# Kernel tuning notes

Hardware: AMD Instinct MI355X
Metric: run time of the kernel (lower is better)

The kernel has to match this reference:

```python
import jax, jax.numpy as jnp
import numpy as np

N = 50000
E = 800000
IN_DIM = 128
HIDDEN = 128
OUT_DIM = 64
NUM_GRAPHS = 64


def setup_inputs() -> dict:
    key = jax.random.key(0)
    ks = jax.random.split(key, 16)
    x = jax.random.normal(ks[0], (N, IN_DIM), dtype=jnp.float32)
    edge_index = jax.random.randint(ks[1], (2, E), 0, N, dtype=jnp.int32)
    batch = jnp.sort(jax.random.randint(ks[2], (N,), 0, NUM_GRAPHS, dtype=jnp.int32))

    def glorot(k, shape):
        fan_in = shape[1]
        return jax.random.normal(k, shape, dtype=jnp.float32) / jnp.sqrt(jnp.float32(fan_in))

    # SAGEConv params: lin_l (on aggregated neighbors, with bias), lin_r (on self, no bias)
    return {
        "x": x,
        "edge_index": edge_index,
        "batch": batch,
        "W1l": glorot(ks[3], (HIDDEN, IN_DIM)), "b1l": jnp.zeros((HIDDEN,), jnp.float32),
        "W1r": glorot(ks[4], (HIDDEN, IN_DIM)),
        "W2l": glorot(ks[5], (HIDDEN, HIDDEN)), "b2l": jnp.zeros((HIDDEN,), jnp.float32),
        "W2r": glorot(ks[6], (HIDDEN, HIDDEN)),
        "W3l": glorot(ks[7], (HIDDEN, HIDDEN)), "b3l": jnp.zeros((HIDDEN,), jnp.float32),
        "W3r": glorot(ks[8], (HIDDEN, HIDDEN)),
        "Wlin": glorot(ks[9], (OUT_DIM, HIDDEN)), "blin": jnp.zeros((OUT_DIM,), jnp.float32),
    }


def sage_conv(x, src, dst, Wl, bl, Wr):
    # aggr='add': scatter-add source features onto target nodes, then two linears.
    agg = jax.ops.segment_sum(x[src], dst, num_segments=N)  # [N, d_in]
    return agg @ Wl.T + bl + x @ Wr.T


def reference(x, edge_index, batch, W1l, b1l, W1r, W2l, b2l, W2r, W3l, b3l, W3r, Wlin, blin):
    src, dst = edge_index[0], edge_index[1]
    h = jax.nn.relu(sage_conv(x, src, dst, W1l, b1l, W1r))
    # dropout p=0.3 is identity at inference
    h = jax.nn.relu(sage_conv(h, src, dst, W2l, b2l, W2r))
    h = sage_conv(h, src, dst, W3l, b3l, W3r)
    # global mean pool over graphs
    sums = jax.ops.segment_sum(h, batch, num_segments=NUM_GRAPHS)  # [G, hidden]
    counts = jax.ops.segment_sum(jnp.ones((N,), h.dtype), batch, num_segments=NUM_GRAPHS)
    pooled = sums / jnp.maximum(counts, 1.0)[:, None]
    return pooled @ Wlin.T + blin  # [G, out_dim]
```

## Files before the change

kernel.cpp:

```cpp
#include <hip/hip_runtime.h>


typedef __bf16 bf16x8 __attribute__((ext_vector_type(8)));
typedef float f32x4 __attribute__((ext_vector_type(4)));
typedef float f32x2 __attribute__((ext_vector_type(2)));

#define BINB 160
#define NBMAX 512

static __device__ __forceinline__ float bf2f(unsigned short u) {
    union { unsigned u; float f; } c; c.u = (unsigned)u << 16; return c.f;
}
static __device__ __forceinline__ unsigned short f2bf(float f) {
    unsigned u = __builtin_bit_cast(unsigned, f);
    return (unsigned short)((u + 0x7fffu + ((u >> 16) & 1u)) >> 16);
}
static __device__ __forceinline__ uint2 pk8_fp8(const float* f) {
    int lo = 0, hi = 0;
    lo = __builtin_amdgcn_cvt_pk_fp8_f32(f[0], f[1], lo, false);
    lo = __builtin_amdgcn_cvt_pk_fp8_f32(f[2], f[3], lo, true);
    hi = __builtin_amdgcn_cvt_pk_fp8_f32(f[4], f[5], hi, false);
    hi = __builtin_amdgcn_cvt_pk_fp8_f32(f[6], f[7], hi, true);
    return make_uint2((unsigned)lo, (unsigned)hi);
}
static __device__ __forceinline__ unsigned char f2fp8(float v) {
    return (unsigned char)(__builtin_amdgcn_cvt_pk_fp8_f32(v, v, 0, false) & 0xff);
}

__global__ __launch_bounds__(256) void k_bincount(
    const int* __restrict__ dst, int* __restrict__ cnt_mat, int E, int nb, int epb)
{
    __shared__ int lc[NBMAX];
    for (int i = threadIdx.x; i < nb; i += 256) lc[i] = 0;
    __syncthreads();
    int b0 = blockIdx.x * epb;
    int b1 = min(b0 + epb, E);
    for (int i = b0 + threadIdx.x; i < b1; i += 256)
        atomicAdd(&lc[dst[i] >> 7], 1);
    __syncthreads();
    for (int i = threadIdx.x; i < nb; i += 256)
        cnt_mat[i * BINB + blockIdx.x] = lc[i];
}

__global__ __launch_bounds__(256) void k_mrowscan(
    const int* __restrict__ cnt_mat, int* __restrict__ rowloc, int* __restrict__ btot)
{
    __shared__ int s[256];
    int b = blockIdx.x;
    int t = threadIdx.x;
    int v = (t < BINB) ? cnt_mat[b * BINB + t] : 0;
    s[t] = v;
    __syncthreads();
#pragma unroll
    for (int off = 1; off < 256; off <<= 1) {
        int u = (t >= off) ? s[t - off] : 0;
        __syncthreads();
        s[t] += u;
        __syncthreads();
    }
    if (t < BINB) rowloc[b * BINB + t] = s[t] - v;
    if (t == 255) btot[b] = s[255];
}

__global__ __launch_bounds__(256) void k_scan2b(
    const int* __restrict__ btot, int* __restrict__ bbase, int nb, int* __restrict__ total_out)
{
    __shared__ int s[256];
    int t = threadIdx.x;
    int per = (nb + 255) / 256;
    int s0 = t * per, e0 = min(s0 + per, nb);
    int sum = 0;
    for (int i = s0; i < e0; ++i) sum += btot[i];
    s[t] = sum;
    __syncthreads();
#pragma unroll
    for (int off = 1; off < 256; off <<= 1) {
        int u = (t >= off) ? s[t - off] : 0;
        __syncthreads();
        s[t] += u;
        __syncthreads();
    }
    int run = s[t] - sum;
    for (int i = s0; i < e0; ++i) { bbase[i] = run; run += btot[i]; }
    if (t == 255) *total_out = s[255];
}

__global__ __launch_bounds__(256) void k_binscatter(
    const int* __restrict__ ei, const int* __restrict__ rowloc, const int* __restrict__ bbase,
    unsigned* __restrict__ binned, int E, int nb, int epb)
{
    __shared__ int lofs[NBMAX];
    __shared__ int lcnt[NBMAX];
    for (int i = threadIdx.x; i < nb; i += 256) {
        lofs[i] = rowloc[i * BINB + blockIdx.x] + bbase[i];
        lcnt[i] = 0;
    }
    __syncthreads();
    int b0 = blockIdx.x * epb;
    int b1 = min(b0 + epb, E);
    for (int i = b0 + threadIdx.x; i < b1; i += 256) {
        int s = ei[i];
        int d = ei[E + i];
        int b = d >> 7;
        int r = atomicAdd(&lcnt[b], 1);
        binned[lofs[b] + r] = (unsigned)s | ((unsigned)(d & 127) << 16);
    }
}

__global__ __launch_bounds__(256) void k_fillfine2(
    const unsigned* __restrict__ binned, const int* __restrict__ bbase,
    int* __restrict__ starts, unsigned short* __restrict__ csr_src,
    int E, int nb, int n)
{
    __shared__ int lc[128];
    __shared__ int lpos[128];
    int b = blockIdx.x;
    int t = threadIdx.x;
    int node0 = b << 7;
    int bs = bbase[b];
    int be = (b == nb - 1) ? E : bbase[b + 1];
    if (t < 128) lc[t] = 0;
    __syncthreads();
    for (int i = bs + t; i < be; i += 256)
        atomicAdd(&lc[(binned[i] >> 16) & 127], 1);
    __syncthreads();
    int v = (t < 128) ? lc[t] : 0;
    if (t < 128) lpos[t] = v;
    __syncthreads();
#pragma unroll
    for (int off = 1; off < 128; off <<= 1) {
        int u = (t >= off && t < 128) ? lpos[t - off] : 0;
        __syncthreads();
        if (t < 128) lpos[t] += u;
        __syncthreads();
    }
    int excl = (t < 128) ? (lpos[t] - v) : 0;
    __syncthreads();
    if (t < 128) {
        int node = node0 + t;
        if (node < n) starts[node] = bs + excl;
        lpos[t] = bs + excl;
    }
    if (b == nb - 1 && t == 0) starts[n] = E;
    __syncthreads();
    for (int i = bs + t; i < be; i += 256) {
        unsigned e = binned[i];
        int slot = atomicAdd(&lpos[(e >> 16) & 127], 1);
        csr_src[slot] = (unsigned short)(e & 0xffffu);
    }
}

__global__ void k_gseg(const int* __restrict__ batch, const int* __restrict__ starts,
                       int* __restrict__ gestart, int n)
{
    int t = threadIdx.x;
    if (t > 64) return;
    int lo = 0, hi = n;
    while (lo < hi) { int m = (lo + hi) >> 1; if (batch[m] < t) lo = m + 1; else hi = m; }
    gestart[t] = starts[lo];
}

__global__ __launch_bounds__(256) void k_cast_all(
    const float* __restrict__ x, unsigned short* __restrict__ xb,
    unsigned char* __restrict__ x8, int n8, int nxblk,
    const float* __restrict__ W1l, const float* __restrict__ W1r,
    const float* __restrict__ W2l, const float* __restrict__ W2r,
    unsigned short* __restrict__ Whi, unsigned short* __restrict__ Wlo)
{
    int bid = blockIdx.x;
    if (bid < nxblk) {
        int i = bid * 256 + threadIdx.x;
        if (i >= n8) return;
        float f[8];
        *(float4*)(f + 0) = *(const float4*)(x + (size_t)i * 8);
        *(float4*)(f + 4) = *(const float4*)(x + (size_t)i * 8 + 4);
        ushort4 oa, ob;
        oa.x = f2bf(f[0]); oa.y = f2bf(f[1]); oa.z = f2bf(f[2]); oa.w = f2bf(f[3]);
        ob.x = f2bf(f[4]); ob.y = f2bf(f[5]); ob.z = f2bf(f[6]); ob.w = f2bf(f[7]);
        int node = i >> 4, c = i & 15;
        size_t dst = (size_t)(node >> 4) * 2048 + (size_t)(c >> 2) * 512
                   + (size_t)((c & 3) * 16 + (node & 15)) * 8;
        *(ushort4*)(xb + dst) = oa;
        *(ushort4*)(xb + dst + 4) = ob;
        *(uint2*)(x8 + (size_t)i * 8) = pk8_fp8(f);
    } else {
        int wb = bid - nxblk;
        int layer = wb >> 7;
        int j = wb & 127;
        int k = threadIdx.x;
        const float* Wl = (layer == 0) ? W1l : W2l;
        const float* Wr = (layer == 0) ? W1r : W2r;
        float w = (k < 128) ? Wl[j * 128 + k] : Wr[j * 128 + k - 128];
        unsigned short hi = f2bf(w);
        float lo = w - bf2f(hi);
        int wv = j >> 5, jj = (j >> 4) & 1, mr = j & 15;
        int s = k >> 5, quad = (k >> 3) & 3, e = k & 7;
        int lane = quad * 16 + mr;
        size_t o = (size_t)layer * 32768
                 + ((size_t)(((wv * 8 + s) * 2 + jj)) * 64 + lane) * 8 + e;
        Whi[o] = hi;
        Wlo[o] = f2bf(lo);
    }
}

#define ACC8(v)                                                         \
    do {                                                                \
        f32x2 p0 = __builtin_amdgcn_cvt_pk_f32_fp8((v).x, false);       \
        f32x2 p1 = __builtin_amdgcn_cvt_pk_f32_fp8((v).x, true);        \
        f32x2 p2 = __builtin_amdgcn_cvt_pk_f32_fp8((v).y, false);       \
        f32x2 p3 = __builtin_amdgcn_cvt_pk_f32_fp8((v).y, true);        \
        a0 += p0.x; a1 += p0.y; a2 += p1.x; a3 += p1.y;                 \
        a4 += p2.x; a5 += p2.y; a6 += p3.x; a7 += p3.y;                 \
    } while (0)

#define ACC_SEG(sbeg, send)                                             \
    for (int base = (sbeg); base < (send); base += 64) {                \
        int cnt = min(64, (send) - base);                               \
        int idx = (base + lane < (send)) ? (int)csr[base + lane] : 0;   \
        int j = 0;                                                      \
        for (; j + 16 <= cnt; j += 16) {                                \
            int s0 = __shfl(idx, j + eg);                               \
            int s1 = __shfl(idx, j + 4 + eg);                           \
            int s2 = __shfl(idx, j + 8 + eg);                           \
            int s3 = __shfl(idx, j + 12 + eg);                          \
            uint2 v0 = *(const uint2*)(hrow + (size_t)s0 * 128);        \
            uint2 v1 = *(const uint2*)(hrow + (size_t)s1 * 128);        \
            uint2 v2 = *(const uint2*)(hrow + (size_t)s2 * 128);        \
            uint2 v3 = *(const uint2*)(hrow + (size_t)s3 * 128);        \
            ACC8(v0);                                                   \
            ACC8(v1);                                                   \
            ACC8(v2);                                                   \
            ACC8(v3);                                                   \
        }                                                               \
        for (; j + 8 <= cnt; j += 8) {                                  \
            int s0 = __shfl(idx, j + eg);                               \
            int s1 = __shfl(idx, j + 4 + eg);                           \
            uint2 v0 = *(const uint2*)(hrow + (size_t)s0 * 128);        \
            uint2 v1 = *(const uint2*)(hrow + (size_t)s1 * 128);        \
            ACC8(v0);                                                   \
            ACC8(v1);                                                   \
        }                                                               \
        for (; j + 4 <= cnt; j += 4) {                                  \
            int s0 = __shfl(idx, j + eg);                               \
            uint2 v0 = *(const uint2*)(hrow + (size_t)s0 * 128);        \
            ACC8(v0);                                                   \
        }                                                               \
        if (j < cnt) {                                                  \
            int k = j + eg;                                             \
            int sm = __shfl(idx, (k < cnt) ? k : (cnt - 1));            \
            uint2 v = *(const uint2*)(hrow + (size_t)sm * 128);         \
            if (k >= cnt) v = make_uint2(0u, 0u);                       \
            ACC8(v);                                                    \
        }                                                               \
    }

#define REDUCE8()                                                       \
    a0 += __shfl_xor(a0, 16); a0 += __shfl_xor(a0, 32);                 \
    a1 += __shfl_xor(a1, 16); a1 += __shfl_xor(a1, 32);                 \
    a2 += __shfl_xor(a2, 16); a2 += __shfl_xor(a2, 32);                 \
    a3 += __shfl_xor(a3, 16); a3 += __shfl_xor(a3, 32);                 \
    a4 += __shfl_xor(a4, 16); a4 += __shfl_xor(a4, 32);                 \
    a5 += __shfl_xor(a5, 16); a5 += __shfl_xor(a5, 32);                 \
    a6 += __shfl_xor(a6, 16); a6 += __shfl_xor(a6, 32);                 \
    a7 += __shfl_xor(a7, 16); a7 += __shfl_xor(a7, 32);

__global__ __launch_bounds__(256) void k_agg(
    const unsigned char* __restrict__ h8, const int* __restrict__ starts,
    const unsigned short* __restrict__ csr, unsigned short* __restrict__ aggf, int n)
{
    int node = blockIdx.x * 4 + (threadIdx.x >> 6);
    int lane = threadIdx.x & 63;
    if (node >= n) return;
    int eg = lane >> 4;
    int fb = lane & 15;
    const unsigned char* hrow = h8 + fb * 8;
    float a0 = 0.f, a1 = 0.f, a2 = 0.f, a3 = 0.f,
          a4 = 0.f, a5 = 0.f, a6 = 0.f, a7 = 0.f;
    int s = starts[node], e = starts[node + 1];

    ACC_SEG(s, e)
    REDUCE8()

    unsigned u0 = (unsigned)f2bf(a0) | ((unsigned)f2bf(a1) << 16);
    unsigned u1 = (unsigned)f2bf(a2) | ((unsigned)f2bf(a3) << 16);
    unsigned u2 = (unsigned)f2bf(a4) | ((unsigned)f2bf(a5) << 16);
    unsigned u3 = (unsigned)f2bf(a6) | ((unsigned)f2bf(a7) << 16);
    if (eg == 0) {
        size_t dst = (size_t)(node >> 4) * 2048 + (size_t)(fb >> 2) * 512
                   + (size_t)((fb & 3) * 16 + (node & 15)) * 8;
        *(uint4*)(aggf + dst) = make_uint4(u0, u1, u2, u3);
    }
}

__global__ __launch_bounds__(256) void k_aggpool(
    const unsigned char* __restrict__ h8, const unsigned short* __restrict__ csr,
    const int* __restrict__ gestart, float* __restrict__ gsumE, int E)
{
    __shared__ float gbuf[4][128];
    int t = threadIdx.x;
    int B0 = blockIdx.x * 256;
    if (B0 >= E) return;
    for (int q = t; q < 512; q += 256) gbuf[q >> 7][q & 127] = 0.f;
    __syncthreads();

    int lo = 0, hi = 63;
    while (lo < hi) { int m = (lo + hi + 1) >> 1; if (gestart[m] <= B0) lo = m; else hi = m - 1; }
    int gblk = lo;

    int wv = t >> 6;
    int lane = t & 63;
    int e0 = B0 + wv * 64;
    if (e0 < E) {
        int e1 = min(e0 + 64, E);
        int eg = lane >> 4;
        int fb = lane & 15;
        const unsigned char* hrow = h8 + fb * 8;

        int g = gblk;
        while (g < 63 && gestart[g + 1] <= e0) ++g;

        float a0 = 0.f, a1 = 0.f, a2 = 0.f, a3 = 0.f,
              a4 = 0.f, a5 = 0.f, a6 = 0.f, a7 = 0.f;
        int cur = e0;
        bool dirty = false;
        while (cur < e1) {
            int gend = gestart[g + 1];
            int send = min(e1, gend);

            ACC_SEG(cur, send)
            dirty = true;
            cur = send;

            if (cur == gend) {
                REDUCE8()
                if (eg == 0) {
                    int gi = g - gblk;
                    if (gi < 4) {
                        float* d = &gbuf[gi][fb * 8];
                        atomicAdd(d + 0, a0); atomicAdd(d + 1, a1);
                        atomicAdd(d + 2, a2); atomicAdd(d + 3, a3);
                        atomicAdd(d + 4, a4); atomicAdd(d + 5, a5);
                        atomicAdd(d + 6, a6); atomicAdd(d + 7, a7);
                    } else {
                        float* d = &gsumE[(size_t)g * 128 + fb * 8];
                        atomicAdd(d + 0, a0); atomicAdd(d + 1, a1);
                        atomicAdd(d + 2, a2); atomicAdd(d + 3, a3);
                        atomicAdd(d + 4, a4); atomicAdd(d + 5, a5);
                        atomicAdd(d + 6, a6); atomicAdd(d + 7, a7);
                    }
                }
                a0 = a1 = a2 = a3 = a4 = a5 = a6 = a7 = 0.f;
                dirty = false;
                ++g;
                while (g < 63 && gestart[g + 1] <= cur) ++g;
            }
        }
        if (dirty) {
            REDUCE8()
            if (eg == 0) {
                int gi = g - gblk;
                if (gi < 4) {
                    float* d = &gbuf[gi][fb * 8];
                    atomicAdd(d + 0, a0); atomicAdd(d + 1, a1);
                    atomicAdd(d + 2, a2); atomicAdd(d + 3, a3);
                    atomicAdd(d + 4, a4); atomicAdd(d + 5, a5);
                    atomicAdd(d + 6, a6); atomicAdd(d + 7, a7);
                } else {
                    float* d = &gsumE[(size_t)g * 128 + fb * 8];
                    atomicAdd(d + 0, a0); atomicAdd(d + 1, a1);
                    atomicAdd(d + 2, a2); atomicAdd(d + 3, a3);
                    atomicAdd(d + 4, a4); atomicAdd(d + 5, a5);
                    atomicAdd(d + 6, a6); atomicAdd(d + 7, a7);
                }
            }
        }
    }
    __syncthreads();
    for (int q = t; q < 512; q += 256) {
        int sl = q >> 7, c = q & 127;
        float v = gbuf[sl][c];
        if (v != 0.f && gblk + sl < 64)
            atomicAdd(&gsumE[(size_t)(gblk + sl) * 128 + c], v);
    }
}

__global__ __launch_bounds__(256) void k_sage(
    const unsigned short* __restrict__ aggf, const unsigned short* __restrict__ hf,
    const unsigned short* __restrict__ Whi, const unsigned short* __restrict__ Wlo,
    const float* __restrict__ bl, unsigned short* __restrict__ outf,
    unsigned char* __restrict__ out8, int n, int do_relu, int do_outf)
{
    int bid = blockIdx.x;
    int pair = bid >> 1;
    int jh = bid & 1;
    int t = threadIdx.x;
    int wv = t >> 6;
    int l = t & 63;
    int quad = l >> 4;
    int mr = l & 15;
    int js = jh * 4 + wv;
    int jbase = js * 16;
    int nb0 = pair * 2;
    int node0 = pair * 32;

    f32x4 acc0 = (f32x4){0.f, 0.f, 0.f, 0.f};
    f32x4 acc1 = (f32x4){0.f, 0.f, 0.f, 0.f};

    const unsigned short* wphi = Whi + (size_t)(js >> 1) * 8192
                               + (size_t)(js & 1) * 512 + (size_t)l * 8;
    const unsigned short* wplo = Wlo + (size_t)(js >> 1) * 8192
                               + (size_t)(js & 1) * 512 + (size_t)l * 8;

    uint4 pb[2][4];
#define SAGE_LOAD(s, b)                                                   \
    do {                                                                  \
        size_t fo = (size_t)(s) * 1024;                                   \
        const unsigned short* ab = ((s) < 4)                              \
            ? (aggf + (size_t)(s) * 512 + (size_t)l * 8)                  \
            : (hf + (size_t)((s) - 4) * 512 + (size_t)l * 8);             \
        pb[b][0] = *(const uint4*)(wphi + fo);                            \
        pb[b][1] = *(const uint4*)(wplo + fo);                            \
        pb[b][2] = *(const uint4*)(ab + (size_t)nb0 * 2048);              \
        pb[b][3] = *(const uint4*)(ab + (size_t)(nb0 + 1) * 2048);        \
    } while (0)

    SAGE_LOAD(0, 0);
    SAGE_LOAD(1, 1);
#pragma unroll
    for (int s = 0; s < 8; ++s) {
        int b = s & 1;
        bf16x8 bh = __builtin_bit_cast(bf16x8, pb[b][0]);
        bf16x8 bo = __builtin_bit_cast(bf16x8, pb[b][1]);
        bf16x8 a0 = __builtin_bit_cast(bf16x8, pb[b][2]);
        bf16x8 a1 = __builtin_bit_cast(bf16x8, pb[b][3]);
        acc0 = __builtin_amdgcn_mfma_f32_16x16x32_bf16(a0, bh, acc0, 0, 0, 0);
        acc0 = __builtin_amdgcn_mfma_f32_16x16x32_bf16(a0, bo, acc0, 0, 0, 0);
        acc1 = __builtin_amdgcn_mfma_f32_16x16x32_bf16(a1, bh, acc1, 0, 0, 0);
        acc1 = __builtin_amdgcn_mfma_f32_16x16x32_bf16(a1, bo, acc1, 0, 0, 0);
        if (s + 2 < 8) SAGE_LOAD(s + 2, b);
    }
#undef SAGE_LOAD

    int col = jbase + mr;
    float bias = bl[col];
    int q2 = (col >> 3) & 3;
    int e2 = col & 7;
    int so = col >> 5;

#pragma unroll
    for (int mi = 0; mi < 2; ++mi) {
        f32x4 a = mi ? acc1 : acc0;
#pragma unroll
        for (int r = 0; r < 4; ++r) {
            int node = node0 + mi * 16 + quad * 4 + r;
            if (node >= n) continue;
            float v = a[r] + bias;
            if (do_relu) v = fmaxf(v, 0.f);
            if (do_outf)
                outf[(size_t)(node >> 4) * 2048 + (size_t)so * 512
                     + (size_t)(q2 * 16 + (node & 15)) * 8 + e2] = f2bf(v);
            out8[(size_t)node * 128 + col] = f2fp8(v);
        }
    }
}

__global__ __launch_bounds__(256) void k_poolh(
    const unsigned char* __restrict__ h8, const int* __restrict__ batch,
    float* __restrict__ gsumP, int n)
{
    int wave = (blockIdx.x * 256 + threadIdx.x) >> 6;
    int lane = threadIdx.x & 63;
    int r0 = wave * 16;
    if (r0 >= n) return;
    int r1 = min(r0 + 16, n);
    int cur = batch[r0];
    float ax = 0.f, ay = 0.f;
    for (int i = r0; i < r1; ++i) {
        int g = batch[i];
        uchar2 v = *(const uchar2*)(h8 + (size_t)i * 128 + lane * 2);
        if (g != cur) {
            atomicAdd(&gsumP[cur * 128 + lane * 2], ax);
            atomicAdd(&gsumP[cur * 128 + lane * 2 + 1], ay);
            ax = 0.f; ay = 0.f; cur = g;
        }
        unsigned pk = (unsigned)v.x | ((unsigned)v.y << 8);
        f32x2 p = __builtin_amdgcn_cvt_pk_f32_fp8((int)pk, false);
        ax += p.x;
        ay += p.y;
    }
    atomicAdd(&gsumP[cur * 128 + lane * 2], ax);
    atomicAdd(&gsumP[cur * 128 + lane * 2 + 1], ay);
}

__global__ __launch_bounds__(128) void k_final(
    const float* __restrict__ gsumE, const float* __restrict__ gsumP,
    const int* __restrict__ batch,
    const float* __restrict__ W3l, const float* __restrict__ b3,
    const float* __restrict__ W3r,
    const float* __restrict__ Wlin, const float* __restrict__ blin,
    float* __restrict__ out, int n)
{
    __shared__ float tmp[128];
    int g = blockIdx.x;
    int t = threadIdx.x;
    int lo = 0, hi = n;
    while (lo < hi) { int m = (lo + hi) >> 1; if (batch[m] < g) lo = m + 1; else hi = m; }
    int lb = lo;
    hi = n;
    while (lo < hi) { int m = (lo + hi) >> 1; if (batch[m] < g + 1) lo = m + 1; else hi = m; }
    int cnt = lo - lb;
    float inv = (cnt > 0) ? 1.f / (float)cnt : 0.f;

    float acc = 0.f;
    for (int k = 0; k < 128; ++k)
        acc += gsumE[g * 128 + k] * W3l[t * 128 + k]
             + gsumP[g * 128 + k] * W3r[t * 128 + k];
    tmp[t] = acc * inv + ((cnt > 0) ? b3[t] : 0.f);
    __syncthreads();

    if (t < 64) {
        float o = 0.f;
        for (int k = 0; k < 128; ++k)
            o += tmp[k] * Wlin[t * 128 + k];
        out[g * 64 + t] = o + blin[t];
    }
}

extern "C" void kernel_launch(void* const* d_in, const int* in_sizes, int n_in,
                              void* d_out, int out_size, void* d_ws, size_t ws_size,
                              hipStream_t stream) {
    const float* x     = (const float*)d_in[0];
    const int*   ei    = (const int*)d_in[1];
    const int*   batch = (const int*)d_in[2];
    const float* W1l = (const float*)d_in[3];
    const float* b1l = (const float*)d_in[4];
    const float* W1r = (const float*)d_in[5];
    const float* W2l = (const float*)d_in[6];
    const float* b2l = (const float*)d_in[7];
    const float* W2r = (const float*)d_in[8];
    const float* W3l = (const float*)d_in[9];
    const float* b3l = (const float*)d_in[10];
    const float* W3r = (const float*)d_in[11];
    const float* Wlin = (const float*)d_in[12];
    const float* blin = (const float*)d_in[13];

    const int N = in_sizes[2];
    const int E = in_sizes[1] / 2;
    const int nb = (N + 127) >> 7;
    const int epb = (E + BINB - 1) / BINB;

    size_t off = 0;
    auto alloc = [&](size_t bytes) {
        void* p = (char*)d_ws + off;
        off += (bytes + 255) & ~(size_t)255;
        return p;
    };
    int* csr_start = (int*)alloc((size_t)(N + 1) * 4);
    int* cnt_mat   = (int*)alloc((size_t)nb * BINB * 4);
    int* rowloc    = (int*)alloc((size_t)nb * BINB * 4);
    int* btot      = (int*)alloc((size_t)NBMAX * 4);
    int* bbase     = (int*)alloc((size_t)NBMAX * 4);
    int* gestart   = (int*)alloc(256);
    unsigned short* csr_src = (unsigned short*)alloc((size_t)E * 2);
    unsigned short* x_bf   = (unsigned short*)alloc((size_t)N * 128 * 2 + 65536);
    unsigned short* hA     = (unsigned short*)alloc((size_t)N * 128 * 2 + 65536);
    unsigned short* agg_bf = (unsigned short*)alloc((size_t)N * 128 * 2 + 65536);
    unsigned char*  h_f8   = (unsigned char*)alloc((size_t)N * 128);
    unsigned short* Whi = (unsigned short*)alloc(2 * 128 * 256 * 2);
    unsigned short* Wlo = (unsigned short*)alloc(2 * 128 * 256 * 2);
    float* gsumE = (float*)alloc((size_t)64 * 128 * 4);
    float* gsumP = (float*)alloc((size_t)64 * 128 * 4);
    (void)ws_size;

    unsigned* binned = (unsigned*)agg_bf;

    hipMemsetAsync(gsumE, 0, (size_t)2 * 64 * 128 * 4, stream);

    k_bincount<<<BINB, 256, 0, stream>>>(ei + E, cnt_mat, E, nb, epb);
    k_mrowscan<<<nb, 256, 0, stream>>>(cnt_mat, rowloc, btot);
    k_scan2b<<<1, 256, 0, stream>>>(btot, bbase, nb, csr_start + N);
    k_binscatter<<<BINB, 256, 0, stream>>>(ei, rowloc, bbase, binned, E, nb, epb);
    k_fillfine2<<<nb, 256, 0, stream>>>(binned, bbase, csr_start, csr_src, E, nb, N);
    k_gseg<<<1, 128, 0, stream>>>(batch, csr_start, gestart, N);

    int n8 = N * 128 / 8;
    int nxblk = (n8 + 255) / 256;
    k_cast_all<<<nxblk + 2 * 128, 256, 0, stream>>>(
        x, x_bf, h_f8, n8, nxblk, W1l, W1r, W2l, W2r, Whi, Wlo);

    int agg_grid = (N + 3) / 4;
    int sage_grid = ((N + 31) / 32) * 2;
    int pool_grid = (((N + 15) / 16) + 3) / 4;
    int aggpool_grid = (E + 255) / 256;

    k_agg<<<agg_grid, 256, 0, stream>>>(h_f8, csr_start, csr_src, agg_bf, N);
    k_sage<<<sage_grid, 256, 0, stream>>>(agg_bf, x_bf, Whi, Wlo, b1l,
                                          hA, h_f8, N, 1, 1);
    k_agg<<<agg_grid, 256, 0, stream>>>(h_f8, csr_start, csr_src, agg_bf, N);
    k_sage<<<sage_grid, 256, 0, stream>>>(agg_bf, hA, Whi + 32768, Wlo + 32768, b2l,
                                          hA, h_f8, N, 1, 0);
    k_aggpool<<<aggpool_grid, 256, 0, stream>>>(h_f8, csr_src, gestart, gsumE, E);
    k_poolh<<<pool_grid, 256, 0, stream>>>(h_f8, batch, gsumP, N);

    k_final<<<64, 128, 0, stream>>>(gsumE, gsumP, batch, W3l, b3l, W3r,
                                    Wlin, blin, (float*)d_out, N);
}
```

Baseline: 268.3 us.

## Drop bf16 hi/lo weight split, fold gseg into fillfine, merge pool kernels

Weights are now stored as a single bf16 copy instead of a hi/lo split pair, which halves the MFMA count and weight loads in k_sage. The weight layout is re-indexed to match. The graph-segment start computation moves into k_fillfine2, removing the k_gseg launch. k_aggpool and k_poolh are merged into one k_tail launch to save a further launch. The cost is lower weight precision (plain bf16), which may increase numerical error.

```diff
diff --git a/kernel.cpp b/kernel.cpp
--- a/kernel.cpp
+++ b/kernel.cpp
@@ -109,7 +109,8 @@
 
 __global__ __launch_bounds__(256) void k_fillfine2(
     const unsigned* __restrict__ binned, const int* __restrict__ bbase,
-    int* __restrict__ starts, unsigned short* __restrict__ csr_src,
+    const int* __restrict__ batch, int* __restrict__ starts,
+    unsigned short* __restrict__ csr_src, int* __restrict__ gestart,
     int E, int nb, int n)
 {
     __shared__ int lc[128];
@@ -138,7 +139,15 @@
     __syncthreads();
     if (t < 128) {
         int node = node0 + t;
-        if (node < n) starts[node] = bs + excl;
+        if (node < n) {
+            int st = bs + excl;
+            starts[node] = st;
+            int bc = batch[node];
+            int bp = (node == 0) ? -1 : batch[node - 1];
+            for (int g = bp + 1; g <= bc; ++g) gestart[g] = st;
+            if (node == n - 1)
+                for (int g = bc + 1; g <= 64; ++g) gestart[g] = E;
+        }
         lpos[t] = bs + excl;
     }
     if (b == nb - 1 && t == 0) starts[n] = E;
@@ -148,16 +157,6 @@
         int slot = atomicAdd(&lpos[(e >> 16) & 127], 1);
         csr_src[slot] = (unsigned short)(e & 0xffffu);
     }
-}
-
-__global__ void k_gseg(const int* __restrict__ batch, const int* __restrict__ starts,
-                       int* __restrict__ gestart, int n)
-{
-    int t = threadIdx.x;
-    if (t > 64) return;
-    int lo = 0, hi = n;
-    while (lo < hi) { int m = (lo + hi) >> 1; if (batch[m] < t) lo = m + 1; else hi = m; }
-    gestart[t] = starts[lo];
 }
 
 __global__ __launch_bounds__(256) void k_cast_all(
@@ -165,7 +164,7 @@
     unsigned char* __restrict__ x8, int n8, int nxblk,
     const float* __restrict__ W1l, const float* __restrict__ W1r,
     const float* __restrict__ W2l, const float* __restrict__ W2r,
-    unsigned short* __restrict__ Whi, unsigned short* __restrict__ Wlo)
+    unsigned short* __restrict__ Whi)
 {
     int bid = blockIdx.x;
     if (bid < nxblk) {
@@ -191,15 +190,11 @@
         const float* Wl = (layer == 0) ? W1l : W2l;
         const float* Wr = (layer == 0) ? W1r : W2r;
         float w = (k < 128) ? Wl[j * 128 + k] : Wr[j * 128 + k - 128];
-        unsigned short hi = f2bf(w);
-        float lo = w - bf2f(hi);
-        int wv = j >> 5, jj = (j >> 4) & 1, mr = j & 15;
+        int js = j >> 4, mr = j & 15;
         int s = k >> 5, quad = (k >> 3) & 3, e = k & 7;
-        int lane = quad * 16 + mr;
         size_t o = (size_t)layer * 32768
-                 + ((size_t)(((wv * 8 + s) * 2 + jj)) * 64 + lane) * 8 + e;
-        Whi[o] = hi;
-        Wlo[o] = f2bf(lo);
+                 + ((size_t)(js * 8 + s) * 64 + quad * 16 + mr) * 8 + e;
+        Whi[o] = f2bf(w);
     }
 }
 
@@ -292,12 +287,40 @@
     }
 }
 
-__global__ __launch_bounds__(256) void k_aggpool(
+__global__ __launch_bounds__(256) void k_tail(
     const unsigned char* __restrict__ h8, const unsigned short* __restrict__ csr,
-    const int* __restrict__ gestart, float* __restrict__ gsumE, int E)
+    const int* __restrict__ gestart, float* __restrict__ gsumE,
+    const int* __restrict__ batch, float* __restrict__ gsumP,
+    int E, int n, int apgrid)
 {
     __shared__ float gbuf[4][128];
     int t = threadIdx.x;
+    if ((int)blockIdx.x >= apgrid) {
+        int wave = ((blockIdx.x - apgrid) * 256 + t) >> 6;
+        int lane = t & 63;
+        int r0 = wave * 16;
+        if (r0 >= n) return;
+        int r1 = min(r0 + 16, n);
+        int cur = batch[r0];
+        float ax = 0.f, ay = 0.f;
+        for (int i = r0; i < r1; ++i) {
+            int g = batch[i];
+            uchar2 v = *(const uchar2*)(h8 + (size_t)i * 128 + lane * 2);
+            if (g != cur) {
+                atomicAdd(&gsumP[cur * 128 + lane * 2], ax);
+                atomicAdd(&gsumP[cur * 128 + lane * 2 + 1], ay);
+                ax = 0.f; ay = 0.f; cur = g;
+            }
+            unsigned pk = (unsigned)v.x | ((unsigned)v.y << 8);
+            f32x2 p = __builtin_amdgcn_cvt_pk_f32_fp8((int)pk, false);
+            ax += p.x;
+            ay += p.y;
+        }
+        atomicAdd(&gsumP[cur * 128 + lane * 2], ax);
+        atomicAdd(&gsumP[cur * 128 + lane * 2 + 1], ay);
+        return;
+    }
+
     int B0 = blockIdx.x * 256;
     if (B0 >= E) return;
     for (int q = t; q < 512; q += 256) gbuf[q >> 7][q & 127] = 0.f;
@@ -386,7 +409,7 @@
 
 __global__ __launch_bounds__(256) void k_sage(
     const unsigned short* __restrict__ aggf, const unsigned short* __restrict__ hf,
-    const unsigned short* __restrict__ Whi, const unsigned short* __restrict__ Wlo,
+    const unsigned short* __restrict__ Whi,
     const float* __restrict__ bl, unsigned short* __restrict__ outf,
     unsigned char* __restrict__ out8, int n, int do_relu, int do_outf)
 {
@@ -406,22 +429,17 @@
     f32x4 acc0 = (f32x4){0.f, 0.f, 0.f, 0.f};
     f32x4 acc1 = (f32x4){0.f, 0.f, 0.f, 0.f};
 
-    const unsigned short* wphi = Whi + (size_t)(js >> 1) * 8192
-                               + (size_t)(js & 1) * 512 + (size_t)l * 8;
-    const unsigned short* wplo = Wlo + (size_t)(js >> 1) * 8192
-                               + (size_t)(js & 1) * 512 + (size_t)l * 8;
-
-    uint4 pb[2][4];
+    const unsigned short* wp = Whi + (size_t)js * 4096 + (size_t)l * 8;
+
+    uint4 pb[2][3];
 #define SAGE_LOAD(s, b)                                                   \
     do {                                                                  \
-        size_t fo = (size_t)(s) * 1024;                                   \
         const unsigned short* ab = ((s) < 4)                              \
             ? (aggf + (size_t)(s) * 512 + (size_t)l * 8)                  \
             : (hf + (size_t)((s) - 4) * 512 + (size_t)l * 8);             \
-        pb[b][0] = *(const uint4*)(wphi + fo);                            \
-        pb[b][1] = *(const uint4*)(wplo + fo);                            \
-        pb[b][2] = *(const uint4*)(ab + (size_t)nb0 * 2048);              \
-        pb[b][3] = *(const uint4*)(ab + (size_t)(nb0 + 1) * 2048);        \
+        pb[b][0] = *(const uint4*)(wp + (size_t)(s) * 512);               \
+        pb[b][1] = *(const uint4*)(ab + (size_t)nb0 * 2048);              \
+        pb[b][2] = *(const uint4*)(ab + (size_t)(nb0 + 1) * 2048);        \
     } while (0)
 
     SAGE_LOAD(0, 0);
@@ -430,13 +448,10 @@
     for (int s = 0; s < 8; ++s) {
         int b = s & 1;
         bf16x8 bh = __builtin_bit_cast(bf16x8, pb[b][0]);
-        bf16x8 bo = __builtin_bit_cast(bf16x8, pb[b][1]);
-        bf16x8 a0 = __builtin_bit_cast(bf16x8, pb[b][2]);
-        bf16x8 a1 = __builtin_bit_cast(bf16x8, pb[b][3]);
+        bf16x8 a0 = __builtin_bit_cast(bf16x8, pb[b][1]);
+        bf16x8 a1 = __builtin_bit_cast(bf16x8, pb[b][2]);
         acc0 = __builtin_amdgcn_mfma_f32_16x16x32_bf16(a0, bh, acc0, 0, 0, 0);
-        acc0 = __builtin_amdgcn_mfma_f32_16x16x32_bf16(a0, bo, acc0, 0, 0, 0);
         acc1 = __builtin_amdgcn_mfma_f32_16x16x32_bf16(a1, bh, acc1, 0, 0, 0);
-        acc1 = __builtin_amdgcn_mfma_f32_16x16x32_bf16(a1, bo, acc1, 0, 0, 0);
         if (s + 2 < 8) SAGE_LOAD(s + 2, b);
     }
 #undef SAGE_LOAD
@@ -462,34 +477,6 @@
             out8[(size_t)node * 128 + col] = f2fp8(v);
         }
     }
-}
-
-__global__ __launch_bounds__(256) void k_poolh(
-    const unsigned char* __restrict__ h8, const int* __restrict__ batch,
-    float* __restrict__ gsumP, int n)
-{
-    int wave = (blockIdx.x * 256 + threadIdx.x) >> 6;
-    int lane = threadIdx.x & 63;
-    int r0 = wave * 16;
-    if (r0 >= n) return;
-    int r1 = min(r0 + 16, n);
-    int cur = batch[r0];
-    float ax = 0.f, ay = 0.f;
-    for (int i = r0; i < r1; ++i) {
-        int g = batch[i];
-        uchar2 v = *(const uchar2*)(h8 + (size_t)i * 128 + lane * 2);
-        if (g != cur) {
-            atomicAdd(&gsumP[cur * 128 + lane * 2], ax);
-            atomicAdd(&gsumP[cur * 128 + lane * 2 + 1], ay);
-            ax = 0.f; ay = 0.f; cur = g;
-        }
-        unsigned pk = (unsigned)v.x | ((unsigned)v.y << 8);
-        f32x2 p = __builtin_amdgcn_cvt_pk_f32_fp8((int)pk, false);
-        ax += p.x;
-        ay += p.y;
-    }
-    atomicAdd(&gsumP[cur * 128 + lane * 2], ax);
-    atomicAdd(&gsumP[cur * 128 + lane * 2 + 1], ay);
 }
 
 __global__ __launch_bounds__(128) void k_final(
@@ -560,14 +547,13 @@
     int* rowloc    = (int*)alloc((size_t)nb * BINB * 4);
     int* btot      = (int*)alloc((size_t)NBMAX * 4);
     int* bbase     = (int*)alloc((size_t)NBMAX * 4);
-    int* gestart   = (int*)alloc(256);
+    int* gestart   = (int*)alloc(256 + 64);
     unsigned short* csr_src = (unsigned short*)alloc((size_t)E * 2);
     unsigned short* x_bf   = (unsigned short*)alloc((size_t)N * 128 * 2 + 65536);
     unsigned short* hA     = (unsigned short*)alloc((size_t)N * 128 * 2 + 65536);
     unsigned short* agg_bf = (unsigned short*)alloc((size_t)N * 128 * 2 + 65536);
     unsigned char*  h_f8   = (unsigned char*)alloc((size_t)N * 128);
     unsigned short* Whi = (unsigned short*)alloc(2 * 128 * 256 * 2);
-    unsigned short* Wlo = (unsigned short*)alloc(2 * 128 * 256 * 2);
     float* gsumE = (float*)alloc((size_t)64 * 128 * 4);
     float* gsumP = (float*)alloc((size_t)64 * 128 * 4);
     (void)ws_size;
@@ -580,13 +566,13 @@
     k_mrowscan<<<nb, 256, 0, stream>>>(cnt_mat, rowloc, btot);
     k_scan2b<<<1, 256, 0, stream>>>(btot, bbase, nb, csr_start + N);
     k_binscatter<<<BINB, 256, 0, stream>>>(ei, rowloc, bbase, binned, E, nb, epb);
-    k_fillfine2<<<nb, 256, 0, stream>>>(binned, bbase, csr_start, csr_src, E, nb, N);
-    k_gseg<<<1, 128, 0, stream>>>(batch, csr_start, gestart, N);
+    k_fillfine2<<<nb, 256, 0, stream>>>(binned, bbase, batch, csr_start, csr_src,
+                                        gestart, E, nb, N);
 
     int n8 = N * 128 / 8;
     int nxblk = (n8 + 255) / 256;
     k_cast_all<<<nxblk + 2 * 128, 256, 0, stream>>>(
-        x, x_bf, h_f8, n8, nxblk, W1l, W1r, W2l, W2r, Whi, Wlo);
+        x, x_bf, h_f8, n8, nxblk, W1l, W1r, W2l, W2r, Whi);
 
     int agg_grid = (N + 3) / 4;
     int sage_grid = ((N + 31) / 32) * 2;
@@ -594,13 +580,13 @@
     int aggpool_grid = (E + 255) / 256;
 
     k_agg<<<agg_grid, 256, 0, stream>>>(h_f8, csr_start, csr_src, agg_bf, N);
-    k_sage<<<sage_grid, 256, 0, stream>>>(agg_bf, x_bf, Whi, Wlo, b1l,
+    k_sage<<<sage_grid, 256, 0, stream>>>(agg_bf, x_bf, Whi, b1l,
                                           hA, h_f8, N, 1, 1);
     k_agg<<<agg_grid, 256, 0, stream>>>(h_f8, csr_start, csr_src, agg_bf, N);
-    k_sage<<<sage_grid, 256, 0, stream>>>(agg_bf, hA, Whi + 32768, Wlo + 32768, b2l,
+    k_sage<<<sage_grid, 256, 0, stream>>>(agg_bf, hA, Whi + 32768, b2l,
                                           hA, h_f8, N, 1, 0);
-    k_aggpool<<<aggpool_grid, 256, 0, stream>>>(h_f8, csr_src, gestart, gsumE, E);
-    k_poolh<<<pool_grid, 256, 0, stream>>>(h_f8, batch, gsumP, N);
+    k_tail<<<aggpool_grid + pool_grid, 256, 0, stream>>>(
+        h_f8, csr_src, gestart, gsumE, batch, gsumP, E, N, aggpool_grid);
 
     k_final<<<64, 128, 0, stream>>>(gsumE, gsumP, batch, W3l, b3l, W3r,
                                     Wlin, blin, (float*)d_out, N);
```

After: 245.8 us. 8.4% less time.
